# Kernel optimization log

Hardware: AMD Instinct MI355X
Metric: run time of the kernel (lower is better)

## Reference

```python
import jax, jax.numpy as jnp
import numpy as np

N, IN_F, OUT_F = 8192, 512, 256
NEG_INF = -9e15
LEAKY_SLOPE = 0.25


def setup_inputs() -> dict:
    key = jax.random.key(0)
    k1, k2, k3, k4, k5, k6 = jax.random.split(key, 6)
    inp = {
        "input": jax.random.normal(k1, (N, IN_F), dtype=jnp.float32),
        "adj": jax.random.randint(k2, (N, N), 0, 2, dtype=jnp.int32),
        # learned params (xavier-normal-ish scale)
        "weights": jax.random.normal(k3, (IN_F, OUT_F), dtype=jnp.float32) * (2.0 / (IN_F + OUT_F)) ** 0.5,
        "a1": jax.random.normal(k4, (OUT_F, 1), dtype=jnp.float32) * (2.0 / (OUT_F + 1)) ** 0.5,
        "a2": jax.random.normal(k5, (OUT_F, 1), dtype=jnp.float32) * (2.0 / (OUT_F + 1)) ** 0.5,
        "bias": jax.random.uniform(k6, (OUT_F,), dtype=jnp.float32, minval=-1.0 / OUT_F ** 0.5, maxval=1.0 / OUT_F ** 0.5),
    }
    return inp


def reference(input, adj, weights, a1, a2, bias):
    # h = input @ W  : [N, out]
    h = input @ weights
    # e[i,j] = leaky_relu((h@a1)[i] + (h@a2)[j])  : [N, N] via broadcast
    e1 = h @ a1  # [N,1]
    e2 = h @ a2  # [N,1]
    e = e1 + e2.T
    e = jnp.where(e > 0, e, LEAKY_SLOPE * e)
    # mask non-edges, row softmax (dropout omitted: deterministic reference)
    scores = jnp.where(adj > 0, e, NEG_INF)
    attention = jax.nn.softmax(scores, axis=1)
    # aggregate + bias
    return attention @ h + bias
```

## Files before the change

kernel.cpp:

```cpp
#include <hip/hip_runtime.h>
#include <hip/hip_fp16.h>

typedef __attribute__((ext_vector_type(8))) short short8;
typedef __attribute__((ext_vector_type(4))) float floatx4;
typedef __attribute__((ext_vector_type(4))) unsigned int uintx4;
typedef __attribute__((ext_vector_type(2))) unsigned int uintx2;
typedef __attribute__((ext_vector_type(4))) int intx4;
typedef __attribute__((ext_vector_type(4))) unsigned short ushortx4;
typedef unsigned int u32;

#define NN 8192
#define KIN 512
#define COUT 256
#define SHIFT 16.0f

#define AS1 __attribute__((address_space(1)))
#define AS3 __attribute__((address_space(3)))

__device__ __forceinline__ void stage16(const void* g, void* l) {
  __builtin_amdgcn_global_load_lds((const AS1 u32*)g, (AS3 u32*)l, 16, 0, 0);
}

__device__ __forceinline__ unsigned int f2bf(float f) {
  unsigned int u = __float_as_uint(f);
  return (u + 0x7FFFu + ((u >> 16) & 1u)) >> 16;
}

__device__ __forceinline__ u32 pkbf(float lo, float hi) {
  u32 a = __float_as_uint(lo) + 0x8000u;
  u32 b = __float_as_uint(hi) + 0x8000u;
  return __builtin_amdgcn_perm(b, a, 0x07060302u);
}

__device__ __forceinline__ short8 pack8(const float* p) {
  uintx4 w;
  w.x = pkbf(p[0], p[1]);
  w.y = pkbf(p[2], p[3]);
  w.z = pkbf(p[4], p[5]);
  w.w = pkbf(p[6], p[7]);
  union { uintx4 u; short8 s; } cv; cv.u = w;
  return cv.s;
}

__global__ __launch_bounds__(256)
void k_prep(const float* __restrict__ in, ushortx4* __restrict__ inA4,
            const float* __restrict__ w, unsigned short* __restrict__ wt) {
  int b = blockIdx.x;
  if (b < 4096) {
    int idx = b * 256 + threadIdx.x;
    floatx4 v = ((const floatx4*)in)[idx];
    ushortx4 o;
    o.x = (unsigned short)f2bf(v.x);
    o.y = (unsigned short)f2bf(v.y);
    o.z = (unsigned short)f2bf(v.z);
    o.w = (unsigned short)f2bf(v.w);
    inA4[idx] = o;
  } else {
    int idx = (b - 4096) * 256 + threadIdx.x;
    int k = idx >> 8, c = idx & 255;
    wt[c * KIN + k] = (unsigned short)f2bf(w[idx]);
  }
}

__global__ __launch_bounds__(128)
void k_gemm_h(const unsigned short* __restrict__ inA, const unsigned short* __restrict__ wt,
              const float* __restrict__ a1, const float* __restrict__ a2,
              unsigned short* __restrict__ ht, float* __restrict__ e1, float* __restrict__ e2,
              float* __restrict__ A1, float* __restrict__ A2, u32* __restrict__ e2pk) {
  int wave = threadIdx.x >> 6;
  int lane = threadIdx.x & 63;
  int n = lane & 15, q = lane >> 4;
  int row0 = blockIdx.x * 32 + wave * 16;
  int mrow = row0 + n;

  floatx4 acc[16];
#pragma unroll
  for (int t = 0; t < 16; ++t) acc[t] = (floatx4){0.f, 0.f, 0.f, 0.f};

  for (int kc = 0; kc < KIN / 32; ++kc) {
    int k0 = kc * 32 + q * 8;
    short8 a = *(const short8*)(inA + (size_t)mrow * KIN + k0);
#pragma unroll
    for (int nt = 0; nt < 16; ++nt) {
      short8 b = *(const short8*)(wt + (size_t)(nt * 16 + n) * KIN + k0);
      acc[nt] = __builtin_amdgcn_mfma_f32_16x16x32_bf16(a, b, acc[nt], 0, 0, 0);
    }
  }

  int i0 = row0 + q * 4;
#pragma unroll
  for (int nt = 0; nt < 16; ++nt) {
    int c = nt * 16 + n;
    uintx2 pk;
    pk.x = f2bf(acc[nt][0]) | (f2bf(acc[nt][1]) << 16);
    pk.y = f2bf(acc[nt][2]) | (f2bf(acc[nt][3]) << 16);
    *(uintx2*)(ht + (size_t)c * NN + i0) = pk;
  }

  float s1[4] = {0.f, 0.f, 0.f, 0.f}, s2[4] = {0.f, 0.f, 0.f, 0.f};
#pragma unroll
  for (int nt = 0; nt < 16; ++nt) {
    float w1 = a1[nt * 16 + n];
    float w2 = a2[nt * 16 + n];
#pragma unroll
    for (int r = 0; r < 4; ++r) {
      s1[r] += acc[nt][r] * w1;
      s2[r] += acc[nt][r] * w2;
    }
  }
#pragma unroll
  for (int m = 1; m < 16; m <<= 1) {
#pragma unroll
    for (int r = 0; r < 4; ++r) {
      s1[r] += __shfl_xor(s1[r], m);
      s2[r] += __shfl_xor(s2[r], m);
    }
  }
  if (n == 0) {
#pragma unroll
    for (int r = 0; r < 4; ++r) {
      float v1 = s1[r], v2 = s2[r];
      e1[i0 + r] = v1;
      e2[i0 + r] = v2;
      A1[i0 + r] = __expf(v1 - 8.0f);
      A2[i0 + r] = __expf(0.25f * v1 - 8.0f);
      u32 b1 = f2bf(__expf(v2 - 8.0f));
      u32 b2 = f2bf(__expf(0.25f * v2 - 8.0f));
      e2pk[i0 + r] = (b1 << 16) | b2;
    }
  }
}

__global__ __launch_bounds__(256, 2)
void k_attn_v4(const int* __restrict__ adj, const unsigned short* __restrict__ ht,
               const float* __restrict__ A1, const float* __restrict__ A2,
               const u32* __restrict__ e2pk,
               __half2* __restrict__ oph, float* __restrict__ Dpart) {
  __shared__ __align__(16) char smem[69632];
  u32* e2s = (u32*)(smem + 65536);

  int b = blockIdx.x;
  int rg = b >> 3, js = b & 7;
  int wave = threadIdx.x >> 6, lane = threadIdx.x & 63;
  int n = lane & 15, q = lane >> 4;
  int rowbase = rg * 128 + wave * 32;
  int jbeg = js * 1024;
  int swz = q ^ ((n >> 1) & 3);

  float A1v0 = A1[rowbase + n],      A2v0 = A2[rowbase + n];
  float A1v1 = A1[rowbase + 16 + n], A2v1 = A2[rowbase + 16 + n];

  floatx4 acc[2][16];
  floatx4 accd[2];
#pragma unroll
  for (int t = 0; t < 2; ++t) {
    accd[t] = (floatx4){0.f, 0.f, 0.f, 0.f};
#pragma unroll
    for (int nt = 0; nt < 16; ++nt) acc[t][nt] = (floatx4){0.f, 0.f, 0.f, 0.f};
  }

  union { uintx4 u; short8 s; } onesu;
  onesu.u = (uintx4){0x3F803F80u, 0x3F803F80u, 0x3F803F80u, 0x3F803F80u};
  short8 ones = onesu.s;

  const int* ar0 = adj + (size_t)(rowbase + n) * NN + jbeg + q * 8;
  const int* ar1 = adj + (size_t)(rowbase + 16 + n) * NN + jbeg + q * 8;

  auto stage = [&](int ch, int buf) {
    int j0g = jbeg + ch * 32;
    char* hbase = smem + buf * 16384;
#pragma unroll
    for (int i = 0; i < 4; ++i) {
      int seg = wave * 256 + i * 64 + lane;
      int c = seg >> 2;
      int o = (seg & 3) ^ ((seg >> 3) & 3);
      stage16(ht + (size_t)c * NN + j0g + o * 8, hbase + (size_t)(wave * 256 + i * 64) * 16);
    }
  };

  intx4 aE[4], aO[4];

  ((uintx4*)e2s)[threadIdx.x] = *(const uintx4*)(e2pk + jbeg + threadIdx.x * 4);
  asm volatile("" ::: "memory");
  stage(0, 0);
  aE[0] = *(const intx4*)(ar0);
  aE[1] = *(const intx4*)(ar0 + 4);
  aE[2] = *(const intx4*)(ar1);
  aE[3] = *(const intx4*)(ar1 + 4);
  asm volatile("" ::: "memory");
  stage(1, 1);
  aO[0] = *(const intx4*)(ar0 + 32);
  aO[1] = *(const intx4*)(ar0 + 36);
  aO[2] = *(const intx4*)(ar1 + 32);
  aO[3] = *(const intx4*)(ar1 + 36);
  asm volatile("s_waitcnt lgkmcnt(0)" ::: "memory");
  asm volatile("s_barrier" ::: "memory");

  auto body = [&](int ch, intx4* aC, int mode) {
    int buf = ch & 3;
    if (mode == 0) stage(ch + 2, (ch + 2) & 3);

    uintx4 ba = *(const uintx4*)(e2s + ch * 32 + q * 8);
    uintx4 bb = *(const uintx4*)(e2s + ch * 32 + q * 8 + 4);
    u32 bw[8] = {ba.x, ba.y, ba.z, ba.w, bb.x, bb.y, bb.z, bb.w};

    float p0[8], p1[8];
#pragma unroll
    for (int jj = 0; jj < 8; ++jj) {
      int av0 = (jj < 4) ? aC[0][jj] : aC[1][jj - 4];
      int av1 = (jj < 4) ? aC[2][jj] : aC[3][jj - 4];
      float B1 = __uint_as_float(bw[jj] & 0xffff0000u);
      float B2 = __uint_as_float(bw[jj] << 16);
      float m10 = A1v0 * B1, m20 = A2v0 * B2;
      float m11 = A1v1 * B1, m21 = A2v1 * B2;
      float pm0 = fmaxf(m10, m20);
      float pm1 = fmaxf(m11, m21);
      p0[jj] = (av0 != 0) ? pm0 : 0.f;
      p1[jj] = (av1 != 0) ? pm1 : 0.f;
    }
    short8 af0 = pack8(p0);
    short8 af1 = pack8(p1);

    if (mode == 0) {
      int jn = (ch + 2) * 32;
      aC[0] = *(const intx4*)(ar0 + jn);
      aC[1] = *(const intx4*)(ar0 + jn + 4);
      aC[2] = *(const intx4*)(ar1 + jn);
      aC[3] = *(const intx4*)(ar1 + jn + 4);
    }

    if (mode == 0)      asm volatile("s_waitcnt vmcnt(16)" ::: "memory");
    else if (mode == 1) asm volatile("s_waitcnt vmcnt(8)" ::: "memory");
    else                asm volatile("s_waitcnt vmcnt(0)" ::: "memory");
    asm volatile("s_barrier" ::: "memory");

    const short8* lb = (const short8*)(smem + (size_t)buf * 16384);
#pragma unroll
    for (int t = 0; t < 16; ++t) {
      short8 bfv = lb[t * 64 + n * 4 + swz];
      acc[0][t] = __builtin_amdgcn_mfma_f32_16x16x32_bf16(af0, bfv, acc[0][t], 0, 0, 0);
      acc[1][t] = __builtin_amdgcn_mfma_f32_16x16x32_bf16(af1, bfv, acc[1][t], 0, 0, 0);
    }
    accd[0] = __builtin_amdgcn_mfma_f32_16x16x32_bf16(af0, ones, accd[0], 0, 0, 0);
    accd[1] = __builtin_amdgcn_mfma_f32_16x16x32_bf16(af1, ones, accd[1], 0, 0, 0);
  };

  for (int ch = 0; ch < 30; ch += 2) {
    body(ch, aE, 0);
    body(ch + 1, aO, 0);
  }
  body(30, aE, 1);
  body(31, aO, 2);

  if (n == 0) {
#pragma unroll
    for (int t2 = 0; t2 < 2; ++t2)
#pragma unroll
      for (int r = 0; r < 4; ++r)
        Dpart[(size_t)js * NN + rowbase + t2 * 16 + q * 4 + r] = accd[t2][r];
  }

#pragma unroll
  for (int t2 = 0; t2 < 2; ++t2) {
    int ibase = rowbase + t2 * 16 + q * 4;
#pragma unroll
    for (int nt = 0; nt < 16; ++nt) {
      int c = nt * 16 + n;
      oph[((size_t)js * 4096 + (ibase >> 1)) * 256 + c] =
          __floats2half2_rn(acc[t2][nt][0], acc[t2][nt][1]);
      oph[((size_t)js * 4096 + (ibase >> 1) + 1) * 256 + c] =
          __floats2half2_rn(acc[t2][nt][2], acc[t2][nt][3]);
    }
  }
}

__global__ void k_final_part(float* __restrict__ out, const __half2* __restrict__ oph,
                             const float* __restrict__ Dpart, const float* __restrict__ bias) {
  int i = blockIdx.x;
  int c = threadIdx.x;
  int hi = i & 1;
  float s = 0.f, d = 0.f;
#pragma unroll
  for (int js = 0; js < 8; ++js) {
    __half2 h2 = oph[((size_t)js * 4096 + (i >> 1)) * 256 + c];
    s += hi ? __high2float(h2) : __low2float(h2);
    d += Dpart[(size_t)js * NN + i];
  }
  out[(size_t)i * COUT + c] = s / fmaxf(d, 1e-37f) + bias[c];
}

__global__ __launch_bounds__(256, 2)
void k_attn_atomic(const int* __restrict__ adj, const unsigned short* __restrict__ ht,
                   const float* __restrict__ e1, const float* __restrict__ e2,
                   float* __restrict__ out_num, float* __restrict__ Dbuf) {
  int b = blockIdx.x;
  int rg = b >> 3, js = b & 7;
  int wave = threadIdx.x >> 6, lane = threadIdx.x & 63;
  int n = lane & 15, q = lane >> 4;
  int rowbase = rg * 128 + wave * 32;

  float e1v0 = e1[rowbase + n];
  float e1v1 = e1[rowbase + 16 + n];

  floatx4 acc[2][16];
#pragma unroll
  for (int t = 0; t < 2; ++t)
#pragma unroll
    for (int nt = 0; nt < 16; ++nt) acc[t][nt] = (floatx4){0.f, 0.f, 0.f, 0.f};

  float d0 = 0.f, d1 = 0.f;
  int jbeg = js * 1024;

  for (int ch = 0; ch < 32; ++ch) {
    int j0 = jbeg + ch * 32 + q * 8;
    floatx4 ea = *(const floatx4*)(e2 + j0);
    floatx4 eb = *(const floatx4*)(e2 + j0 + 4);
    float ev[8] = {ea.x, ea.y, ea.z, ea.w, eb.x, eb.y, eb.z, eb.w};

    intx4 A00 = *(const intx4*)(adj + (size_t)(rowbase + n) * NN + j0);
    intx4 A01 = *(const intx4*)(adj + (size_t)(rowbase + n) * NN + j0 + 4);
    intx4 A10 = *(const intx4*)(adj + (size_t)(rowbase + 16 + n) * NN + j0);
    intx4 A11 = *(const intx4*)(adj + (size_t)(rowbase + 16 + n) * NN + j0 + 4);

    float p0[8], p1[8];
#pragma unroll
    for (int jj = 0; jj < 8; ++jj) {
      int av0 = (jj < 4) ? A00[jj] : A01[jj - 4];
      int av1 = (jj < 4) ? A10[jj] : A11[jj - 4];
      float t0 = e1v0 + ev[jj];
      float t1 = e1v1 + ev[jj];
      float f0 = fmaxf(t0, 0.25f * t0);
      float f1 = fmaxf(t1, 0.25f * t1);
      float x0 = __expf(f0 - SHIFT);
      float x1 = __expf(f1 - SHIFT);
      p0[jj] = (av0 != 0) ? x0 : 0.f;
      p1[jj] = (av1 != 0) ? x1 : 0.f;
      d0 += p0[jj];
      d1 += p1[jj];
    }
    short8 af0 = pack8(p0);
    short8 af1 = pack8(p1);

#pragma unroll
    for (int g = 0; g < 2; ++g) {
      short8 bf[8];
#pragma unroll
      for (int t = 0; t < 8; ++t)
        bf[t] = *(const short8*)(ht + (size_t)((g * 8 + t) * 16 + n) * NN + j0);
#pragma unroll
      for (int t = 0; t < 8; ++t) {
        acc[0][g * 8 + t] = __builtin_amdgcn_mfma_f32_16x16x32_bf16(af0, bf[t], acc[0][g * 8 + t], 0, 0, 0);
        acc[1][g * 8 + t] = __builtin_amdgcn_mfma_f32_16x16x32_bf16(af1, bf[t], acc[1][g * 8 + t], 0, 0, 0);
      }
    }
  }

  d0 += __shfl_xor(d0, 16); d0 += __shfl_xor(d0, 32);
  d1 += __shfl_xor(d1, 16); d1 += __shfl_xor(d1, 32);
  if (lane < 16) {
    atomicAdd(Dbuf + rowbase + lane, d0);
    atomicAdd(Dbuf + rowbase + 16 + lane, d1);
  }

#pragma unroll
  for (int t2 = 0; t2 < 2; ++t2) {
#pragma unroll
    for (int nt = 0; nt < 16; ++nt) {
#pragma unroll
      for (int r = 0; r < 4; ++r) {
        int i = rowbase + t2 * 16 + q * 4 + r;
        atomicAdd(out_num + (size_t)i * COUT + nt * 16 + n, acc[t2][nt][r]);
      }
    }
  }
}

__global__ void k_final_atomic(float* __restrict__ out, const float* __restrict__ Dbuf,
                               const float* __restrict__ bias) {
  int idx = blockIdx.x * 256 + threadIdx.x;
  int i = idx >> 8, c = idx & 255;
  float d = fmaxf(Dbuf[i], 1e-37f);
  out[idx] = out[idx] / d + bias[c];
}

extern "C" void kernel_launch(void* const* d_in, const int* in_sizes, int n_in,
                              void* d_out, int out_size, void* d_ws, size_t ws_size,
                              hipStream_t stream) {
  const float* input   = (const float*)d_in[0];
  const int*   adj     = (const int*)d_in[1];
  const float* weights = (const float*)d_in[2];
  const float* a1      = (const float*)d_in[3];
  const float* a2      = (const float*)d_in[4];
  const float* bias    = (const float*)d_in[5];
  float* out = (float*)d_out;
  char* ws = (char*)d_ws;

  unsigned short* inA = (unsigned short*)(ws);
  unsigned short* wt  = (unsigned short*)(ws + 8388608);
  unsigned short* ht  = (unsigned short*)(ws + 8650752);
  float* e1    = (float*)(ws + 12845056);
  float* e2    = (float*)(ws + 12877824);
  float* A1    = (float*)(ws + 12910592);
  float* A2    = (float*)(ws + 12943360);
  u32*   e2pk  = (u32*)  (ws + 12976128);
  float* Dpart = (float*)(ws + 13008896);
  __half2* oph = (__half2*)(ws + 13271040);
  const size_t WS_NEEDED_PART = 13271040 + (size_t)8 * NN * COUT * 2;
  float* Dbuf = Dpart;

  k_prep<<<4608, 256, 0, stream>>>(input, (ushortx4*)inA, weights, wt);
  k_gemm_h<<<256, 128, 0, stream>>>(inA, wt, a1, a2, ht, e1, e2, A1, A2, e2pk);

  if (ws_size >= WS_NEEDED_PART) {
    k_attn_v4<<<512, 256, 0, stream>>>(adj, ht, A1, A2, e2pk, oph, Dpart);
    k_final_part<<<8192, 256, 0, stream>>>(out, oph, Dpart, bias);
  } else {
    hipMemsetAsync(out, 0, (size_t)NN * COUT * sizeof(float), stream);
    hipMemsetAsync(Dbuf, 0, NN * sizeof(float), stream);
    k_attn_atomic<<<512, 256, 0, stream>>>(adj, ht, e1, e2, out, Dbuf);
    k_final_atomic<<<8192, 256, 0, stream>>>(out, Dbuf, bias);
  }
}
```

Measured before the change: 446.0 us.

## Prefetch adjacency in four-chunk groups with deeper double-buffered register pipeline

The attention kernel now loads adjacency rows for four 32-column chunks at once into two register banks (gA/gB), issuing the next group's loads mid-group, rather than loading one chunk two steps ahead. The hand-written vmcnt wait counts and the LDS stage indexing are reworked to match the new schedule. The aim is to keep more global loads in flight to hide the latency of the large adjacency stream. The cost is higher VGPR pressure from 32 intx4 registers, which could cause spills or lower occupancy under launch_bounds(256,2), and the manual wait counts must line up exactly.

```diff
diff --git a/kernel.cpp b/kernel.cpp
--- a/kernel.cpp
+++ b/kernel.cpp
@@ -132,7 +132,7 @@
 }
 
 __global__ __launch_bounds__(256, 2)
-void k_attn_v4(const int* __restrict__ adj, const unsigned short* __restrict__ ht,
+void k_attn_v6(const int* __restrict__ adj, const unsigned short* __restrict__ ht,
                const float* __restrict__ A1, const float* __restrict__ A2,
                const u32* __restrict__ e2pk,
                __half2* __restrict__ oph, float* __restrict__ Dpart) {
@@ -178,27 +178,32 @@
     }
   };
 
-  intx4 aE[4], aO[4];
-
-  ((uintx4*)e2s)[threadIdx.x] = *(const uintx4*)(e2pk + jbeg + threadIdx.x * 4);
+  intx4 gA[16], gB[16];
+
+  auto ldgroup = [&](int g, intx4* arr) {
+    const int* b0 = ar0 + g * 128;
+    const int* b1 = ar1 + g * 128;
+#pragma unroll
+    for (int k = 0; k < 4; ++k) {
+      arr[k * 4 + 0] = *(const intx4*)(b0 + k * 32);
+      arr[k * 4 + 1] = *(const intx4*)(b0 + k * 32 + 4);
+      arr[k * 4 + 2] = *(const intx4*)(b1 + k * 32);
+      arr[k * 4 + 3] = *(const intx4*)(b1 + k * 32 + 4);
+    }
+  };
+
+  uintx4 ev = *(const uintx4*)(e2pk + jbeg + threadIdx.x * 4);
+  ((uintx4*)e2s)[threadIdx.x] = ev;
   asm volatile("" ::: "memory");
   stage(0, 0);
-  aE[0] = *(const intx4*)(ar0);
-  aE[1] = *(const intx4*)(ar0 + 4);
-  aE[2] = *(const intx4*)(ar1);
-  aE[3] = *(const intx4*)(ar1 + 4);
-  asm volatile("" ::: "memory");
   stage(1, 1);
-  aO[0] = *(const intx4*)(ar0 + 32);
-  aO[1] = *(const intx4*)(ar0 + 36);
-  aO[2] = *(const intx4*)(ar1 + 32);
-  aO[3] = *(const intx4*)(ar1 + 36);
+  ldgroup(0, gA);
   asm volatile("s_waitcnt lgkmcnt(0)" ::: "memory");
   asm volatile("s_barrier" ::: "memory");
 
-  auto body = [&](int ch, intx4* aC, int mode) {
-    int buf = ch & 3;
-    if (mode == 0) stage(ch + 2, (ch + 2) & 3);
+  auto body = [&](int ch, int k, intx4* aC, int wcnt, bool doStage, int gNext, intx4* aN) {
+    if (doStage) stage(ch + 2, (k + 2) & 3);
+    if (gNext >= 0) ldgroup(gNext, aN);
 
     uintx4 ba = *(const uintx4*)(e2s + ch * 32 + q * 8);
     uintx4 bb = *(const uintx4*)(e2s + ch * 32 + q * 8 + 4);
@@ -207,8 +212,8 @@
     float p0[8], p1[8];
 #pragma unroll
     for (int jj = 0; jj < 8; ++jj) {
-      int av0 = (jj < 4) ? aC[0][jj] : aC[1][jj - 4];
-      int av1 = (jj < 4) ? aC[2][jj] : aC[3][jj - 4];
+      int av0 = (jj < 4) ? aC[k * 4 + 0][jj] : aC[k * 4 + 1][jj - 4];
+      int av1 = (jj < 4) ? aC[k * 4 + 2][jj] : aC[k * 4 + 3][jj - 4];
       float B1 = __uint_as_float(bw[jj] & 0xffff0000u);
       float B2 = __uint_as_float(bw[jj] << 16);
       float m10 = A1v0 * B1, m20 = A2v0 * B2;
@@ -221,20 +226,13 @@
     short8 af0 = pack8(p0);
     short8 af1 = pack8(p1);
 
-    if (mode == 0) {
-      int jn = (ch + 2) * 32;
-      aC[0] = *(const intx4*)(ar0 + jn);
-      aC[1] = *(const intx4*)(ar0 + jn + 4);
-      aC[2] = *(const intx4*)(ar1 + jn);
-      aC[3] = *(const intx4*)(ar1 + jn + 4);
-    }
-
-    if (mode == 0)      asm volatile("s_waitcnt vmcnt(16)" ::: "memory");
-    else if (mode == 1) asm volatile("s_waitcnt vmcnt(8)" ::: "memory");
-    else                asm volatile("s_waitcnt vmcnt(0)" ::: "memory");
+    if (wcnt == 24)      asm volatile("s_waitcnt vmcnt(24)" ::: "memory");
+    else if (wcnt == 8)  asm volatile("s_waitcnt vmcnt(8)" ::: "memory");
+    else if (wcnt == 4)  asm volatile("s_waitcnt vmcnt(4)" ::: "memory");
+    else                 asm volatile("s_waitcnt vmcnt(0)" ::: "memory");
     asm volatile("s_barrier" ::: "memory");
 
-    const short8* lb = (const short8*)(smem + (size_t)buf * 16384);
+    const short8* lb = (const short8*)(smem + (size_t)k * 16384);
 #pragma unroll
     for (int t = 0; t < 16; ++t) {
       short8 bfv = lb[t * 64 + n * 4 + swz];
@@ -245,12 +243,23 @@
     accd[1] = __builtin_amdgcn_mfma_f32_16x16x32_bf16(af1, ones, accd[1], 0, 0, 0);
   };
 
-  for (int ch = 0; ch < 30; ch += 2) {
-    body(ch, aE, 0);
-    body(ch + 1, aO, 0);
-  }
-  body(30, aE, 1);
-  body(31, aO, 2);
+  body(0, 0, gA, 4,  true, -1, nullptr);
+  body(1, 1, gA, 8,  true, -1, nullptr);
+  body(2, 2, gA, 24, true, 1, gB);
+  body(3, 3, gA, 24, true, -1, nullptr);
+  for (int g = 1; g < 7; ++g) {
+    int ch = g * 4;
+    intx4* C = (g & 1) ? gB : gA;
+    intx4* Nx = (g & 1) ? gA : gB;
+    body(ch + 0, 0, C, 8,  true, -1, nullptr);
+    body(ch + 1, 1, C, 8,  true, -1, nullptr);
+    body(ch + 2, 2, C, 24, true, g + 1, Nx);
+    body(ch + 3, 3, C, 24, true, -1, nullptr);
+  }
+  body(28, 0, gB, 8, true,  -1, nullptr);
+  body(29, 1, gB, 8, true,  -1, nullptr);
+  body(30, 2, gB, 4, false, -1, nullptr);
+  body(31, 3, gB, 0, false, -1, nullptr);
 
   if (n == 0) {
 #pragma unroll
@@ -412,7 +421,7 @@
   k_gemm_h<<<256, 128, 0, stream>>>(inA, wt, a1, a2, ht, e1, e2, A1, A2, e2pk);
 
   if (ws_size >= WS_NEEDED_PART) {
-    k_attn_v4<<<512, 256, 0, stream>>>(adj, ht, A1, A2, e2pk, oph, Dpart);
+    k_attn_v6<<<512, 256, 0, stream>>>(adj, ht, A1, A2, e2pk, oph, Dpart);
     k_final_part<<<8192, 256, 0, stream>>>(out, oph, Dpart, bias);
   } else {
     hipMemsetAsync(out, 0, (size_t)NN * COUT * sizeof(float), stream);
```

After: 867.0 us. 94.4% more time.
